# Performance work log

Hardware: AMD Instinct MI355X
Metric: run time of the kernel (lower is better)

## Reference

```python
import jax, jax.numpy as jnp
import numpy as np
import math

B, T, C = 4, 2048, 1024
NH = 16
HD = C // NH


def setup_inputs() -> dict:
    key = jax.random.key(0)
    ks = jax.random.split(key, 10)
    s = 0.02
    x = jax.random.normal(ks[0], (B, T, C), dtype=jnp.float32)
    W_qkv = jax.random.normal(ks[1], (C, 3 * C), dtype=jnp.float32) * s
    b_qkv = jnp.zeros((3 * C,), dtype=jnp.float32)
    W_proj = jax.random.normal(ks[2], (C, C), dtype=jnp.float32) * s
    b_proj = jnp.zeros((C,), dtype=jnp.float32)
    asym_mean, asym_std = 1.0, 0.7
    q_scale = jax.random.normal(ks[3], (NH, HD), dtype=jnp.float32) * asym_std + asym_mean
    q_bias = jax.random.normal(ks[4], (NH, HD), dtype=jnp.float32) * asym_std + asym_mean
    k_scale = jax.random.normal(ks[5], (NH, HD), dtype=jnp.float32) * asym_std + asym_mean
    k_bias = jax.random.normal(ks[6], (NH, HD), dtype=jnp.float32) * asym_std + asym_mean
    return {"x": x, "W_qkv": W_qkv, "b_qkv": b_qkv, "W_proj": W_proj,
            "b_proj": b_proj, "q_scale": q_scale, "q_bias": q_bias,
            "k_scale": k_scale, "k_bias": k_bias}


def reference(x, W_qkv, b_qkv, W_proj, b_proj, q_scale, q_bias, k_scale, k_bias):
    Bx, Tx, Cx = x.shape
    qkv = x @ W_qkv + b_qkv                       # [B,T,3C]
    q, k, v = jnp.split(qkv, 3, axis=-1)
    # [B,T,C] -> [B,NH,T,HD]
    reshape = lambda t: t.reshape(Bx, Tx, NH, HD).transpose(0, 2, 1, 3)
    q, k, v = reshape(q), reshape(k), reshape(v)
    # per-head affine scaling of Q/K
    q = q * q_scale[None, :, None, :] + q_bias[None, :, None, :]
    k = k * k_scale[None, :, None, :] + k_bias[None, :, None, :]
    scores = jnp.einsum('bhqd,bhkd->bhqk', q, k) / math.sqrt(HD)  # [B,NH,T,T]
    causal = jnp.tril(jnp.ones((Tx, Tx), dtype=bool))
    scores = jnp.where(causal[None, None], scores, -jnp.inf)
    att = jax.nn.softmax(scores, axis=-1)
    y = jnp.einsum('bhqk,bhkd->bhqd', att, v)     # [B,NH,T,HD]
    y = y.transpose(0, 2, 1, 3).reshape(Bx, Tx, Cx)
    return y @ W_proj + b_proj
```

## Files before the change

### kernel.cpp

```cpp
#include <hip/hip_runtime.h>
#include <hip/hip_bf16.h>

typedef unsigned short u16;
typedef __attribute__((ext_vector_type(8))) short short8;
typedef __attribute__((ext_vector_type(4))) float floatx4;

#define B_SZ 4
#define T_SZ 2048
#define C_SZ 1024
#define NH_SZ 16
#define HD_SZ 64
#define M_TOT 8192
#define K_DIM 1024

#define QSCALE 0.1803368801111204f

#define OFF_XB   ((size_t)16)
#define OFF_WQT  (OFF_XB + 8388608)
#define OFF_WPT  (OFF_WQT + 3145728)
#define OFF_PB   (OFF_WPT + 1048576)
#define OFF_Q    (OFF_PB + 8192)
#define OFF_K    (OFF_Q + 8388608)
#define OFF_V    (OFF_K + 8388608)
#define OFF_Y    (OFF_V + 8388608)
#define PB_BQKV  0
#define PB_BPROJ 3072
#define PB_QSC   4096
#define PB_QBI   5120
#define PB_KSC   6144
#define PB_KBI   7168

__device__ __forceinline__ float bf2f(u16 u) {
    return __uint_as_float(((unsigned)u) << 16);
}
__device__ __forceinline__ u16 f2bf(float f) {
    unsigned x = __float_as_uint(f);
    unsigned r = (x + 0x7fffu + ((x >> 16) & 1u)) >> 16;
    return (u16)r;
}
__device__ __forceinline__ u16 f2bf_fast(float f) {
    return (u16)((__float_as_uint(f) + 0x8000u) >> 16);
}
__device__ __forceinline__ unsigned cvt_pk_bf16(float lo, float hi) {
    unsigned r;
    asm("v_cvt_pk_bf16_f32 %0, %1, %2" : "=v"(r) : "v"(lo), "v"(hi));
    return r;
}
__device__ __forceinline__ void gl_lds16(const u16* g, u16* l) {
    __builtin_amdgcn_global_load_lds(
        (const __attribute__((address_space(1))) void*)g,
        (__attribute__((address_space(3))) void*)l, 16, 0, 0);
}
__device__ __forceinline__ int detect_isf(const u16* xx, int lane) {
    float v0 = fabsf(bf2f(xx[lane * 2]));
    float v1 = fabsf(bf2f(xx[lane * 2 + 1]));
    int b0 = (v0 > 1024.0f) || (v0 != 0.0f && v0 < 9.5367431640625e-7f);
    int b1 = (v1 > 1024.0f) || (v1 != 0.0f && v1 < 9.5367431640625e-7f);
    unsigned long long ba = __ballot(b0), bb = __ballot(b1);
    return (__popcll(ba) + __popcll(bb)) > 8;
}

__global__ __launch_bounds__(256) void prep_k(
        const void* __restrict__ x,
        const void* __restrict__ Wqkv, const void* __restrict__ Wproj,
        const void* __restrict__ bqkv, const void* __restrict__ bproj,
        const void* __restrict__ qsc, const void* __restrict__ qbi,
        const void* __restrict__ ksc, const void* __restrict__ kbi,
        u16* __restrict__ xb, u16* __restrict__ Wt_qkv,
        u16* __restrict__ Wt_proj, u16* __restrict__ pb,
        int* __restrict__ flag) {
    __shared__ u16 t[32][36];
    const int blk = blockIdx.x;
    const int isf = detect_isf((const u16*)x, threadIdx.x & 63);
    if (blk == 0 && threadIdx.x == 0) flag[0] = isf;
    if (blk < 8192) {
        const int i = blk * 256 + threadIdx.x;
        if (isf) {
            const float4 v = ((const float4*)x)[i];
            ushort4 o;
            o.x = f2bf(v.x); o.y = f2bf(v.y); o.z = f2bf(v.z); o.w = f2bf(v.w);
            ((ushort4*)xb)[i] = o;
        } else {
            ((ushort4*)xb)[i] = ((const ushort4*)x)[i];
        }
        return;
    }
    if (blk < 8200) {
        const int i4 = (blk - 8192) * 256 + threadIdx.x;
        if (i4 >= 2048) return;
        const int e = i4 * 4;
        const void* src; int off;
        if (e < 3072)      { src = bqkv;  off = e; }
        else if (e < 4096) { src = bproj; off = e - 3072; }
        else if (e < 5120) { src = qsc;   off = e - 4096; }
        else if (e < 6144) { src = qbi;   off = e - 5120; }
        else if (e < 7168) { src = ksc;   off = e - 6144; }
        else               { src = kbi;   off = e - 7168; }
        ushort4 o;
        if (isf) {
            const float4 v = *(const float4*)((const float*)src + off);
            o.x = f2bf(v.x); o.y = f2bf(v.y); o.z = f2bf(v.z); o.w = f2bf(v.w);
        } else {
            o = *(const ushort4*)((const u16*)src + off);
        }
        *(ushort4*)&pb[e] = o;
        return;
    }
    const void* in; u16* out; int R, C, idx;
    if (blk < 11272) { idx = blk - 8200;  in = Wqkv;  out = Wt_qkv;  R = 1024; C = 3072; }
    else             { idx = blk - 11272; in = Wproj; out = Wt_proj; R = 1024; C = 1024; }
    const int nbx = C >> 5;
    const int c0 = (idx % nbx) * 32, r0 = (idx / nbx) * 32;
    {
        const int r = threadIdx.x >> 3, cq = threadIdx.x & 7;
        const size_t gi = (size_t)(r0 + r) * C + c0 + cq * 4;
        ushort4 v4;
        if (isf) {
            const float4 v = *(const float4*)((const float*)in + gi);
            v4.x = f2bf(v.x); v4.y = f2bf(v.y); v4.z = f2bf(v.z); v4.w = f2bf(v.w);
        } else {
            v4 = *(const ushort4*)((const u16*)in + gi);
        }
        *(ushort4*)&t[r][cq * 4] = v4;
    }
    __syncthreads();
    {
        const int cr = threadIdx.x & 31, g = threadIdx.x >> 5;
        ushort4 o;
        o.x = t[g * 4 + 0][cr]; o.y = t[g * 4 + 1][cr];
        o.z = t[g * 4 + 2][cr]; o.w = t[g * 4 + 3][cr];
        *(ushort4*)&out[(size_t)(c0 + cr) * R + r0 + g * 4] = o;
    }
}

#define QG_BM 256
#define QG_BN 192
#define QG_NT 16

__global__ __launch_bounds__(512, 2) void qkv_gemm(
        const u16* __restrict__ X, const u16* __restrict__ Wt,
        const u16* __restrict__ pb,
        u16* __restrict__ Qb, u16* __restrict__ Kb, u16* __restrict__ Vb) {
    __shared__ __align__(16) u16 As[2][QG_BM * 64];
    __shared__ __align__(16) u16 Bs[2][QG_BN * 64];
    const int bm = blockIdx.y * QG_BM, bn = blockIdx.x * QG_BN;
    const int tid = threadIdx.x;
    const int lane = tid & 63, w = tid >> 6;
    const int quad = lane >> 4, l16 = lane & 15;
    const int wm = (w & 3) * 64;
    const int wn = (w >> 2) * 96;
    const int lrow = lane >> 3;
    const int lcol = ((lane & 7) ^ lrow) * 8;
    const int sl0 = ((0 + quad) ^ (l16 & 7)) * 8;
    const int sl1 = ((4 + quad) ^ (l16 & 7)) * 8;

#define QG_STAGE(slot, kt) do {                                                  \
        const int k0_ = (kt) * 64;                                               \
        _Pragma("unroll")                                                        \
        for (int j = 0; j < 4; j++) {                                            \
            const int rb = w * 32 + j * 8;                                       \
            gl_lds16(&X[(size_t)(bm + rb + lrow) * K_DIM + k0_ + lcol],          \
                     &As[slot][rb * 64]);                                        \
        }                                                                        \
        _Pragma("unroll")                                                        \
        for (int j = 0; j < 3; j++) {                                            \
            const int rb = w * 24 + j * 8;                                       \
            gl_lds16(&Wt[(size_t)(bn + rb + lrow) * K_DIM + k0_ + lcol],         \
                     &Bs[slot][rb * 64]);                                        \
        }                                                                        \
    } while (0)

    floatx4 acc[4][6];
#pragma unroll
    for (int mi = 0; mi < 4; mi++)
#pragma unroll
        for (int ni = 0; ni < 6; ni++) acc[mi][ni] = 0.f;

    QG_STAGE(0, 0);
    QG_STAGE(1, 1);
    asm volatile("s_waitcnt vmcnt(7)" ::: "memory");
    __builtin_amdgcn_s_barrier();

    for (int t = 0; t < QG_NT; ++t) {
        const int cur = t & 1;
        const u16* as = As[cur];
        const u16* bs = Bs[cur];
        short8 a[4], b[6];
#pragma unroll
        for (int mi = 0; mi < 4; mi++)
            a[mi] = *(const short8*)&as[(wm + mi * 16 + l16) * 64 + sl0];
#pragma unroll
        for (int ni = 0; ni < 6; ni++)
            b[ni] = *(const short8*)&bs[(wn + ni * 16 + l16) * 64 + sl0];
        __builtin_amdgcn_s_setprio(1);
#pragma unroll
        for (int mi = 0; mi < 4; mi++)
#pragma unroll
            for (int ni = 0; ni < 6; ni++)
                acc[mi][ni] = __builtin_amdgcn_mfma_f32_16x16x32_bf16(
                    a[mi], b[ni], acc[mi][ni], 0, 0, 0);
        __builtin_amdgcn_s_setprio(0);
#pragma unroll
        for (int mi = 0; mi < 4; mi++)
            a[mi] = *(const short8*)&as[(wm + mi * 16 + l16) * 64 + sl1];
#pragma unroll
        for (int ni = 0; ni < 6; ni++)
            b[ni] = *(const short8*)&bs[(wn + ni * 16 + l16) * 64 + sl1];
        asm volatile("s_waitcnt lgkmcnt(0)" ::: "memory");
        __builtin_amdgcn_s_barrier();
        if (t < QG_NT - 1) {
            const int tn = (t + 2 < QG_NT) ? t + 2 : QG_NT - 1;
            QG_STAGE(cur, tn);
        }
        __builtin_amdgcn_s_setprio(1);
#pragma unroll
        for (int mi = 0; mi < 4; mi++)
#pragma unroll
            for (int ni = 0; ni < 6; ni++)
                acc[mi][ni] = __builtin_amdgcn_mfma_f32_16x16x32_bf16(
                    a[mi], b[ni], acc[mi][ni], 0, 0, 0);
        __builtin_amdgcn_s_setprio(0);
        asm volatile("s_waitcnt vmcnt(7)" ::: "memory");
        __builtin_amdgcn_s_barrier();
    }
#undef QG_STAGE

    const int bb = bm >> 11;
    const int tbase = bm & 2047;
#pragma unroll
    for (int ni = 0; ni < 6; ni++) {
        const int col = bn + wn + ni * 16 + l16;
        const int sec = col >> 10;
        const int cmod = col & 1023;
        const int h = cmod >> 6, d = cmod & 63;
        const float bv = bf2f(pb[PB_BQKV + col]);
        if (sec == 2) {
#pragma unroll
            for (int mi = 0; mi < 4; mi++) {
                const int t0 = tbase + wm + mi * 16 + quad * 4;
                ushort4 pk;
                pk.x = f2bf(acc[mi][ni][0] + bv);
                pk.y = f2bf(acc[mi][ni][1] + bv);
                pk.z = f2bf(acc[mi][ni][2] + bv);
                pk.w = f2bf(acc[mi][ni][3] + bv);
                *(ushort4*)&Vb[(((size_t)(bb * NH_SZ + h)) * HD_SZ + d) * T_SZ + t0] = pk;
            }
        } else {
            float sA, sB;
            if (sec == 0) {
                sA = bf2f(pb[PB_QSC + h * 64 + d]) * QSCALE;
                sB = bf2f(pb[PB_QBI + h * 64 + d]) * QSCALE;
            } else {
                sA = bf2f(pb[PB_KSC + h * 64 + d]);
                sB = bf2f(pb[PB_KBI + h * 64 + d]);
            }
            u16* dstbuf = (sec == 0) ? Qb : Kb;
#pragma unroll
            for (int mi = 0; mi < 4; mi++)
#pragma unroll
                for (int r = 0; r < 4; r++) {
                    const int tt = tbase + wm + mi * 16 + quad * 4 + r;
                    float v = (acc[mi][ni][r] + bv) * sA + sB;
                    dstbuf[(((size_t)(bb * NH_SZ + h)) * T_SZ + tt) * HD_SZ + d] = f2bf(v);
                }
        }
    }
}

__global__ __launch_bounds__(512, 6) void attn_k(const u16* __restrict__ Qb,
                                                 const u16* __restrict__ Kb,
                                                 const u16* __restrict__ Vtg,
                                                 u16* __restrict__ Y) {
    __shared__ __align__(16) u16 Ks[2][64 * 64];
    __shared__ __align__(16) u16 Vs[2][64 * 64];
    __shared__ __align__(16) u16 Ps[8 * 16 * 72];
    const int blk = blockIdx.x;
    const int head = blk & 63;
    const int qt = 15 - (blk >> 6);
    const int b = head >> 4, h = head & 15;
    const int tid = threadIdx.x, lane = tid & 63, w = tid >> 6;
    const int quad = lane >> 4, l16 = lane & 15;
    const size_t qk_off = (size_t)head * (T_SZ * HD_SZ);
    const size_t v_off = (size_t)head * (HD_SZ * T_SZ);
    u16* psw = &Ps[w * 1152];
    const int lr = lane >> 3;
    const int lc = ((lane & 7) ^ lr) * 8;
    const int sl0 = ((quad) ^ (l16 & 7)) * 8;
    const int sl1 = ((4 + quad) ^ (l16 & 7)) * 8;

    short8 ones;
    for (int j = 0; j < 8; j++) ones[j] = (short)0x3F80;

    const int q0 = qt * 128;
    const int rbase = q0 + w * 16;
    const int q = rbase + l16;
    const int nt = (q0 >> 6) + 2;

    const short8 aq0 = *(const short8*)&Qb[qk_off + (size_t)q * HD_SZ + quad * 8];
    const short8 aq1 = *(const short8*)&Qb[qk_off + (size_t)q * HD_SZ + 32 + quad * 8];

    floatx4 o[4];
    for (int mi = 0; mi < 4; mi++) o[mi] = 0.f;
    float m_run = -1e30f, l_run = 0.f;

    gl_lds16(&Kb[qk_off + (size_t)(w * 8 + lr) * HD_SZ + lc], &Ks[0][w * 512]);
    gl_lds16(&Vtg[v_off + (size_t)(w * 8 + lr) * T_SZ + lc], &Vs[0][w * 512]);

    for (int t = 0; t < nt; ++t) {
        const int cur = t & 1;
        const int k0 = t * 64;
        if (t + 1 < nt) {
            const int kn = k0 + 64;
            gl_lds16(&Kb[qk_off + (size_t)(kn + w * 8 + lr) * HD_SZ + lc],
                     &Ks[cur ^ 1][w * 512]);
            gl_lds16(&Vtg[v_off + (size_t)(w * 8 + lr) * T_SZ + kn + lc],
                     &Vs[cur ^ 1][w * 512]);
            asm volatile("s_waitcnt vmcnt(2)" ::: "memory");
        } else {
            asm volatile("s_waitcnt vmcnt(0)" ::: "memory");
        }
        __builtin_amdgcn_s_barrier();

        if (k0 <= rbase + 15) {
            const u16* ks = Ks[cur];
            const u16* vs = Vs[cur];
            floatx4 s[4];
            for (int ni = 0; ni < 4; ni++) s[ni] = 0.f;
            __builtin_amdgcn_s_setprio(1);
            for (int ni = 0; ni < 4; ni++)
                s[ni] = __builtin_amdgcn_mfma_f32_16x16x32_bf16(
                    *(const short8*)&ks[(ni * 16 + l16) * 64 + sl0], aq0, s[ni], 0, 0, 0);
            for (int ni = 0; ni < 4; ni++)
                s[ni] = __builtin_amdgcn_mfma_f32_16x16x32_bf16(
                    *(const short8*)&ks[(ni * 16 + l16) * 64 + sl1], aq1, s[ni], 0, 0, 0);
            __builtin_amdgcn_s_setprio(0);

            if (k0 + 63 > rbase) {
                for (int ni = 0; ni < 4; ni++)
                    for (int r = 0; r < 4; r++) {
                        int key = k0 + ni * 16 + quad * 4 + r;
                        if (key > q) s[ni][r] = -1e30f;
                    }
            }

            float t0 = fmaxf(fmaxf(s[0][0], s[0][1]), s[0][2]);
            float t1 = fmaxf(fmaxf(s[0][3], s[1][0]), s[1][1]);
            float t2 = fmaxf(fmaxf(s[1][2], s[1][3]), s[2][0]);
            float t3 = fmaxf(fmaxf(s[2][1], s[2][2]), s[2][3]);
            float t4 = fmaxf(fmaxf(s[3][0], s[3][1]), s[3][2]);
            float mx = fmaxf(fmaxf(fmaxf(t0, t1), fmaxf(t2, t3)),
                             fmaxf(t4, s[3][3]));
            mx = fmaxf(mx, __shfl_xor(mx, 16, 64));
            mx = fmaxf(mx, __shfl_xor(mx, 32, 64));

            if (!__all(mx <= m_run + 8.0f)) {
                const float mnew = fmaxf(m_run, mx);
                const float alpha = exp2f(m_run - mnew);
                m_run = mnew;
                for (int mi = 0; mi < 4; mi++) o[mi] *= alpha;
                l_run *= alpha;
            }
            for (int ni = 0; ni < 4; ni++)
                for (int r = 0; r < 4; r++)
                    s[ni][r] = exp2f(s[ni][r] - m_run);

            for (int ni = 0; ni < 4; ni++) {
                uint2 pp;
                pp.x = cvt_pk_bf16(s[ni][0], s[ni][1]);
                pp.y = cvt_pk_bf16(s[ni][2], s[ni][3]);
                *(uint2*)&psw[l16 * 72 + ni * 16 + quad * 4] = pp;
            }

            floatx4 s4 = 0.f;
            __builtin_amdgcn_s_setprio(1);
            for (int kk = 0; kk < 64; kk += 32) {
                short8 pfr = *(const short8*)&psw[l16 * 72 + kk + quad * 8];
                const int vsl = (kk == 0) ? sl0 : sl1;
                s4 = __builtin_amdgcn_mfma_f32_16x16x32_bf16(ones, pfr, s4, 0, 0, 0);
                for (int mi = 0; mi < 4; mi++) {
                    short8 vfr = *(const short8*)&vs[(mi * 16 + l16) * 64 + vsl];
                    o[mi] = __builtin_amdgcn_mfma_f32_16x16x32_bf16(vfr, pfr, o[mi], 0, 0, 0);
                }
            }
            __builtin_amdgcn_s_setprio(0);
            l_run += s4[0];
        }
        asm volatile("s_waitcnt lgkmcnt(0)" ::: "memory");
        __builtin_amdgcn_s_barrier();
    }

    const float inv = 1.0f / l_run;
    u16* yrow = &Y[(((size_t)b * T_SZ + q) * NH_SZ + h) * HD_SZ];
    for (int mi = 0; mi < 4; mi++) {
        uint2 pk2;
        pk2.x = cvt_pk_bf16(o[mi][0] * inv, o[mi][1] * inv);
        pk2.y = cvt_pk_bf16(o[mi][2] * inv, o[mi][3] * inv);
        *(uint2*)&yrow[mi * 16 + quad * 4] = pk2;
    }
}

#define PG_NT 16

__global__ __launch_bounds__(512, 4) void proj_gemm(const u16* __restrict__ Yin,
                                                    const u16* __restrict__ Wt,
                                                    const u16* __restrict__ pb,
                                                    void* __restrict__ out,
                                                    const int* __restrict__ flag) {
    __shared__ __align__(16) u16 As[2][128 * 64];
    __shared__ __align__(16) u16 Bs[2][128 * 64];
    const int isf = flag[0];
    const int bm = blockIdx.y * 128, bn = blockIdx.x * 128;
    const int tid = threadIdx.x;
    const int lane = tid & 63, w = tid >> 6;
    const int quad = lane >> 4, l16 = lane & 15;
    const int wm = (w & 3) * 32, wn = (w >> 2) * 64;
    const int lrow = lane >> 3;
    const int lcol = ((lane & 7) ^ lrow) * 8;
    const int sl0 = ((0 + quad) ^ (l16 & 7)) * 8;
    const int sl1 = ((4 + quad) ^ (l16 & 7)) * 8;

#define PG_STAGE(slot, kt) do {                                                  \
        const int k0_ = (kt) * 64;                                               \
        _Pragma("unroll")                                                        \
        for (int j = 0; j < 2; j++) {                                            \
            const int rb = w * 16 + j * 8;                                       \
            gl_lds16(&Yin[(size_t)(bm + rb + lrow) * K_DIM + k0_ + lcol],        \
                     &As[slot][rb * 64]);                                        \
            gl_lds16(&Wt[(size_t)(bn + rb + lrow) * K_DIM + k0_ + lcol],         \
                     &Bs[slot][rb * 64]);                                        \
        }                                                                        \
    } while (0)

    floatx4 acc[2][4];
#pragma unroll
    for (int mi = 0; mi < 2; mi++)
#pragma unroll
        for (int ni = 0; ni < 4; ni++) acc[mi][ni] = 0.f;

    PG_STAGE(0, 0);
    PG_STAGE(1, 1);
    asm volatile("s_waitcnt vmcnt(4)" ::: "memory");
    __builtin_amdgcn_s_barrier();

    for (int t = 0; t < PG_NT; ++t) {
        const int cur = t & 1;
        const u16* as = As[cur];
        const u16* bs = Bs[cur];
        short8 a[2], b[4];
#pragma unroll
        for (int mi = 0; mi < 2; mi++)
            a[mi] = *(const short8*)&as[(wm + mi * 16 + l16) * 64 + sl0];
#pragma unroll
        for (int ni = 0; ni < 4; ni++)
            b[ni] = *(const short8*)&bs[(wn + ni * 16 + l16) * 64 + sl0];
        __builtin_amdgcn_s_setprio(1);
#pragma unroll
        for (int mi = 0; mi < 2; mi++)
#pragma unroll
            for (int ni = 0; ni < 4; ni++)
                acc[mi][ni] = __builtin_amdgcn_mfma_f32_16x16x32_bf16(
                    a[mi], b[ni], acc[mi][ni], 0, 0, 0);
        __builtin_amdgcn_s_setprio(0);
#pragma unroll
        for (int mi = 0; mi < 2; mi++)
            a[mi] = *(const short8*)&as[(wm + mi * 16 + l16) * 64 + sl1];
#pragma unroll
        for (int ni = 0; ni < 4; ni++)
            b[ni] = *(const short8*)&bs[(wn + ni * 16 + l16) * 64 + sl1];
        asm volatile("s_waitcnt lgkmcnt(0)" ::: "memory");
        __builtin_amdgcn_s_barrier();
        if (t < PG_NT - 1) {
            const int tn = (t + 2 < PG_NT) ? t + 2 : PG_NT - 1;
            PG_STAGE(cur, tn);
        }
        __builtin_amdgcn_s_setprio(1);
#pragma unroll
        for (int mi = 0; mi < 2; mi++)
#pragma unroll
            for (int ni = 0; ni < 4; ni++)
                acc[mi][ni] = __builtin_amdgcn_mfma_f32_16x16x32_bf16(
                    a[mi], b[ni], acc[mi][ni], 0, 0, 0);
        __builtin_amdgcn_s_setprio(0);
        asm volatile("s_waitcnt vmcnt(4)" ::: "memory");
        __builtin_amdgcn_s_barrier();
    }
#undef PG_STAGE

    for (int mi = 0; mi < 2; mi++) {
        for (int ni = 0; ni < 4; ni++) {
            const int col = bn + wn + ni * 16 + l16;
            const float bv = bf2f(pb[PB_BPROJ + col]);
            for (int r = 0; r < 4; r++) {
                const int row = bm + wm + mi * 16 + quad * 4 + r;
                const float v = acc[mi][ni][r] + bv;
                if (isf) ((float*)out)[(size_t)row * C_SZ + col] = v;
                else     ((u16*)out)[(size_t)row * C_SZ + col] = f2bf(v);
            }
        }
    }
}

extern "C" void kernel_launch(void* const* d_in, const int* in_sizes, int n_in,
                              void* d_out, int out_size, void* d_ws, size_t ws_size,
                              hipStream_t stream) {
    const void* x     = d_in[0];
    const void* Wqkv  = d_in[1];
    const void* bqkv  = d_in[2];
    const void* Wproj = d_in[3];
    const void* bproj = d_in[4];
    const void* qsc   = d_in[5];
    const void* qbi   = d_in[6];
    const void* ksc   = d_in[7];
    const void* kbi   = d_in[8];

    u16* ws = (u16*)d_ws;
    int* flag    = (int*)d_ws;
    u16* xb      = ws + OFF_XB;
    u16* Wt_qkv  = ws + OFF_WQT;
    u16* Wt_proj = ws + OFF_WPT;
    u16* pb      = ws + OFF_PB;
    u16* Qb      = ws + OFF_Q;
    u16* Kb      = ws + OFF_K;
    u16* Vb      = ws + OFF_V;
    u16* Yb      = ws + OFF_Y;

    prep_k<<<12296, 256, 0, stream>>>(x, Wqkv, Wproj, bqkv, bproj,
                                      qsc, qbi, ksc, kbi,
                                      xb, Wt_qkv, Wt_proj, pb, flag);
    qkv_gemm<<<dim3(16, 32), 512, 0, stream>>>(xb, Wt_qkv, pb, Qb, Kb, Vb);
    attn_k<<<dim3(1024), 512, 0, stream>>>(Qb, Kb, Vb, Yb);
    proj_gemm<<<dim3(8, 64), 512, 0, stream>>>(Yb, Wt_proj, pb, d_out, flag);
}
```

Baseline: 286.5 us.

## Remap QKV GEMM blocks across XCDs and simplify weight transpose tiles

The QKV GEMM moves from a 2D grid to a 1D grid with a block-id remap. Consecutive hardware block ids (round-robin across the 8 XCDs) now map to contiguous output tiles per XCD, which should improve L2 reuse of the A/B panels. Separately, the weight-transpose part of the prep kernel swaps vectorized ushort4 loads and stores for scalar per-element accesses with a 33-wide padded LDS tile. That narrows global memory transactions, which could slow the prep step.

```diff
diff --git a/kernel.cpp b/kernel.cpp
--- a/kernel.cpp
+++ b/kernel.cpp
@@ -69,7 +69,7 @@
         u16* __restrict__ xb, u16* __restrict__ Wt_qkv,
         u16* __restrict__ Wt_proj, u16* __restrict__ pb,
         int* __restrict__ flag) {
-    __shared__ u16 t[32][36];
+    __shared__ u16 t[32][33];
     const int blk = blockIdx.x;
     const int isf = detect_isf((const u16*)x, threadIdx.x & 63);
     if (blk == 0 && threadIdx.x == 0) flag[0] = isf;
@@ -111,25 +111,16 @@
     else             { idx = blk - 11272; in = Wproj; out = Wt_proj; R = 1024; C = 1024; }
     const int nbx = C >> 5;
     const int c0 = (idx % nbx) * 32, r0 = (idx / nbx) * 32;
-    {
-        const int r = threadIdx.x >> 3, cq = threadIdx.x & 7;
-        const size_t gi = (size_t)(r0 + r) * C + c0 + cq * 4;
-        ushort4 v4;
-        if (isf) {
-            const float4 v = *(const float4*)((const float*)in + gi);
-            v4.x = f2bf(v.x); v4.y = f2bf(v.y); v4.z = f2bf(v.z); v4.w = f2bf(v.w);
-        } else {
-            v4 = *(const ushort4*)((const u16*)in + gi);
-        }
-        *(ushort4*)&t[r][cq * 4] = v4;
+    const int tx = threadIdx.x & 31, ty = threadIdx.x >> 5;
+    for (int i = 0; i < 4; i++) {
+        int r = ty + i * 8;
+        size_t gi = (size_t)(r0 + r) * C + c0 + tx;
+        t[r][tx] = isf ? f2bf(((const float*)in)[gi]) : ((const u16*)in)[gi];
     }
     __syncthreads();
-    {
-        const int cr = threadIdx.x & 31, g = threadIdx.x >> 5;
-        ushort4 o;
-        o.x = t[g * 4 + 0][cr]; o.y = t[g * 4 + 1][cr];
-        o.z = t[g * 4 + 2][cr]; o.w = t[g * 4 + 3][cr];
-        *(ushort4*)&out[(size_t)(c0 + cr) * R + r0 + g * 4] = o;
+    for (int i = 0; i < 4; i++) {
+        int cr = ty + i * 8;
+        out[(size_t)(c0 + cr) * R + r0 + tx] = t[tx][cr];
     }
 }
 
@@ -143,7 +134,8 @@
         u16* __restrict__ Qb, u16* __restrict__ Kb, u16* __restrict__ Vb) {
     __shared__ __align__(16) u16 As[2][QG_BM * 64];
     __shared__ __align__(16) u16 Bs[2][QG_BN * 64];
-    const int bm = blockIdx.y * QG_BM, bn = blockIdx.x * QG_BN;
+    const int wgid = (blockIdx.x & 7) * 64 + (blockIdx.x >> 3);
+    const int bm = (wgid >> 4) * QG_BM, bn = (wgid & 15) * QG_BN;
     const int tid = threadIdx.x;
     const int lane = tid & 63, w = tid >> 6;
     const int quad = lane >> 4, l16 = lane & 15;
@@ -527,7 +519,7 @@
     prep_k<<<12296, 256, 0, stream>>>(x, Wqkv, Wproj, bqkv, bproj,
                                       qsc, qbi, ksc, kbi,
                                       xb, Wt_qkv, Wt_proj, pb, flag);
-    qkv_gemm<<<dim3(16, 32), 512, 0, stream>>>(xb, Wt_qkv, pb, Qb, Kb, Vb);
+    qkv_gemm<<<dim3(512), 512, 0, stream>>>(xb, Wt_qkv, pb, Qb, Kb, Vb);
     attn_k<<<dim3(1024), 512, 0, stream>>>(Qb, Kb, Vb, Yb);
     proj_gemm<<<dim3(8, 64), 512, 0, stream>>>(Yb, Wt_proj, pb, d_out, flag);
 }
```

After: 277.3 us (median of 2 runs). 3.2% less time.
